# Kernel optimization log

Hardware: AMD Instinct MI355X
Metric: run time of the kernel (lower is better)

Reference implementation:

```python
import jax, jax.numpy as jnp
import numpy as np

B, N, OBS, HID, H = 8, 1024, 64, 192, 3
D = HID // H  # head_dim = 64
ALPHA = 0.2   # LeakyReLU negative slope
NEG = -9e15   # mask value from torch code (-9000000000000000.0)


def gat_layer(h, adj, W, a):
    """Multi-head GAT layer, math-identical to the torch per-head loop.
    h: (B,N,F_in), adj: (N,N), W: (H,F_in,D), a: (H,2D).
    Concat-score a^T [Wh_i || Wh_j] is split into a_l^T Wh_i + a_r^T Wh_j
    (broadcast-add) to avoid materializing the N^2 x 2D tensor.
    """
    Wh = jnp.einsum('bni,hid->bhnd', h, W)           # (B,H,N,D)
    d = Wh.shape[-1]
    s_i = jnp.einsum('bhnd,hd->bhn', Wh, a[:, :d])   # a_l . Wh_i
    s_j = jnp.einsum('bhnd,hd->bhn', Wh, a[:, d:])   # a_r . Wh_j
    e = s_i[..., :, None] + s_j[..., None, :]        # (B,H,N,N)
    e = jnp.where(e > 0, e, ALPHA * e)               # LeakyReLU
    e = jnp.where(adj > 0, e, NEG)                   # adjacency mask
    attn = jax.nn.softmax(e, axis=-1)                # (dropout=0 in eval)
    out = jnp.einsum('bhnm,bhmd->bhnd', attn, Wh)    # weighted aggregate
    b, nh, n, _ = out.shape
    return out.transpose(0, 2, 1, 3).reshape(b, n, nh * d)  # concat heads


def setup_inputs() -> dict:
    key = jax.random.key(0)
    k1, k2, k3, k4, k5 = jax.random.split(key, 5)
    h = jax.random.normal(k1, (B, N, OBS), dtype=jnp.float32)
    adj = jnp.ones((N, N), dtype=jnp.float32)  # graph_type='full'
    # xavier_uniform-style scale (gain=1.414)
    def xav(k, shape, fan_in, fan_out):
        lim = 1.414 * np.sqrt(6.0 / (fan_in + fan_out))
        return jax.random.uniform(k, shape, jnp.float32, -lim, lim)
    W1 = xav(k2, (H, OBS, D), OBS, D)
    a1 = xav(k3, (H, 2 * D), 2 * D, 1)
    W2 = xav(k4, (H, HID, D), HID, D)
    a2 = xav(k5, (H, 2 * D), 2 * D, 1)
    return {"h": h, "adj": adj, "W1": W1, "a1": a1, "W2": W2, "a2": a2}


def reference(h, adj, W1, a1, W2, a2):
    x = gat_layer(h, adj, W1, a1)   # (B,N,HID)
    x = jax.nn.elu(x)               # inter-layer nonlinearity
    x = gat_layer(x, adj, W2, a2)   # (B,N,HID)
    return x
```

## Files before the change

### kernel.cpp

```cpp
#include <hip/hip_runtime.h>
#include <math.h>

#define Bc   8
#define Nc   1024
#define OBSc 64
#define HIDc 192
#define NHc  3
#define Dc   64
#define ALPHAc 0.2f

typedef __attribute__((ext_vector_type(8))) _Float16 half8;
typedef __attribute__((ext_vector_type(4))) float floatx4;

__device__ __forceinline__ unsigned int enc_f32(float f) {
    unsigned int u = __float_as_uint(f);
    return (u & 0x80000000u) ? ~u : (u | 0x80000000u);
}
__device__ __forceinline__ float dec_f32(unsigned int e) {
    return __uint_as_float((e & 0x80000000u) ? (e & 0x7FFFFFFFu) : ~e);
}


__global__ __launch_bounds__(256) void proj1_kernel(
    const float* __restrict__ xin,
    const float* __restrict__ W1,
    const float* __restrict__ a,
    _Float16* __restrict__ WhT,
    float* __restrict__ si, float* __restrict__ sj,
    unsigned int* __restrict__ Menc,
    const float* __restrict__ adj,
    unsigned long long* __restrict__ adjb,
    const float* __restrict__ W2,
    _Float16* __restrict__ W2T)
{
    const int tid = threadIdx.x;
    const int bh  = blockIdx.y;

    if (bh == Bc * NHc) {
        const int px = blockIdx.x, wv = tid >> 6, lane = tid & 63;
        for (int r8 = 0; r8 < 8; ++r8) {
            const int i = px * 32 + wv * 8 + r8;
            unsigned long long word = 0;
            for (int g = 0; g < 16; ++g) {
                bool c = adj[(size_t)i * Nc + g * 64 + lane] > 0.f;
                unsigned long long bal = __ballot(c);
                if (lane == g) word = bal;
            }
            if (lane < 16) adjb[(size_t)i * 16 + lane] = word;
        }
        if (px < 12) {
            for (int e = px * 3072 + tid; e < px * 3072 + 3072; e += 256) {
                int t = e & 7, ln = (e >> 3) & 63, p = (e >> 9) & 1, nh = (e >> 10) & 1;
                int g = e >> 11; int ks = g % 6, hh = g / 6;
                int k = ks * 32 + (ln >> 4) * 8 + t;
                int d = nh * 32 + p * 16 + (ln & 15);
                W2T[e] = (_Float16)W2[((size_t)hh * HIDc + k) * Dc + d];
            }
        }
        return;
    }

    __shared__ union {
        _Float16 Bs[64][OBSc + 8];
        _Float16 Ts[64][40];
    } u;
    __shared__ float spsA_i[32], spsA_j[32], spsB_i[32], spsB_j[32];

    const int b = bh / NHc, hh = bh % NHc;
    const int row0 = blockIdx.x * 32;

    for (int e = tid; e < OBSc * 64; e += 256) {
        int k = e >> 6, d = e & 63;
        u.Bs[d][k] = (_Float16)W1[(size_t)hh * OBSc * 64 + e];
    }
    __syncthreads();

    const int lane = tid & 63, wv = tid >> 6;
    const int mblk = (wv & 1) * 16, nhalf = (wv >> 1) * 32;
    const int fr = lane & 15, fq = lane >> 4;
    floatx4 acc0 = {0.f,0.f,0.f,0.f}, acc1 = {0.f,0.f,0.f,0.f};
    const int row = row0 + mblk + fr;

#pragma unroll
    for (int ks = 0; ks < OBSc / 32; ++ks) {
        const int k0 = ks * 32 + fq * 8;
        const float* xr = xin + ((size_t)b * Nc + row) * OBSc + k0;
        float4 u0 = *(const float4*)xr;
        float4 u1 = *(const float4*)(xr + 4);
        half8 af;
        af[0] = (_Float16)u0.x; af[1] = (_Float16)u0.y;
        af[2] = (_Float16)u0.z; af[3] = (_Float16)u0.w;
        af[4] = (_Float16)u1.x; af[5] = (_Float16)u1.y;
        af[6] = (_Float16)u1.z; af[7] = (_Float16)u1.w;
        half8 b0 = *(const half8*)&u.Bs[nhalf + fr][k0];
        half8 b1 = *(const half8*)&u.Bs[nhalf + 16 + fr][k0];
        acc0 = __builtin_amdgcn_mfma_f32_16x16x32_f16(af, b0, acc0, 0, 0, 0);
        acc1 = __builtin_amdgcn_mfma_f32_16x16x32_f16(af, b1, acc1, 0, 0, 0);
    }

    const float al0 = a[hh * 2 * Dc + nhalf + fr];
    const float al1 = a[hh * 2 * Dc + nhalf + 16 + fr];
    const float ar0 = a[hh * 2 * Dc + Dc + nhalf + fr];
    const float ar1 = a[hh * 2 * Dc + Dc + nhalf + 16 + fr];
    float pi[4], pj[4];
#pragma unroll
    for (int r = 0; r < 4; ++r) {
        pi[r] = acc0[r] * al0 + acc1[r] * al1;
        pj[r] = acc0[r] * ar0 + acc1[r] * ar1;
        for (int off = 8; off >= 1; off >>= 1) {
            pi[r] += __shfl_xor(pi[r], off, 64);
            pj[r] += __shfl_xor(pj[r], off, 64);
        }
    }
    if (fr == 0) {
#pragma unroll
        for (int r = 0; r < 4; ++r) {
            int lr = mblk + fq * 4 + r;
            if (nhalf == 0) { spsA_i[lr] = pi[r]; spsA_j[lr] = pj[r]; }
            else            { spsB_i[lr] = pi[r]; spsB_j[lr] = pj[r]; }
        }
    }
    __syncthreads();
    if (tid < 64) {
        float vj = -INFINITY;
        if (tid < 32) {
            size_t g = (size_t)bh * Nc + row0 + tid;
            si[g] = spsA_i[tid] + spsB_i[tid];
            vj    = spsA_j[tid] + spsB_j[tid];
            sj[g] = vj;
        }
        float mv = vj;
        for (int off = 32; off >= 1; off >>= 1) mv = fmaxf(mv, __shfl_xor(mv, off, 64));
        if (tid == 0) atomicMax(&Menc[bh], enc_f32(mv));
    }

#pragma unroll
    for (int nt = 0; nt < 2; ++nt) {
        const int d = nhalf + nt * 16 + fr;
        floatx4 acc = nt ? acc1 : acc0;
#pragma unroll
        for (int p = 0; p < 2; ++p) {
            union { unsigned int w; _Float16 h[2]; } pk;
            pk.h[0] = (_Float16)acc[2 * p];
            pk.h[1] = (_Float16)acc[2 * p + 1];
            *(unsigned int*)&u.Ts[d][mblk + fq * 4 + 2 * p] = pk.w;
        }
    }
    __syncthreads();
    {
        const int c2 = tid >> 6, lane2 = tid & 63;
        const int fr2 = lane2 & 15, fq2 = lane2 >> 4;
        const int jt = row0 >> 5;
        uint4 v = *(const uint4*)&u.Ts[c2 * 16 + fr2][fq2 * 8];
        *(uint4*)&WhT[(size_t)(bh * 32 + jt) * 2048 + tid * 8] = v;
    }
}

__global__ __launch_bounds__(256) void proj2_kernel(
    const _Float16* __restrict__ xh,
    const _Float16* __restrict__ W2T,
    const float* __restrict__ a,
    _Float16* __restrict__ WhT,
    float* __restrict__ si, float* __restrict__ sj,
    unsigned int* __restrict__ Menc)
{
    __shared__ _Float16 Ts[64][40];
    __shared__ float spsA_i[32], spsA_j[32], spsB_i[32], spsB_j[32];

    const int tid = threadIdx.x, bh = blockIdx.y;
    const int b = bh / NHc, hh = bh % NHc;
    const int row0 = blockIdx.x * 32;
    const int lane = tid & 63, wv = tid >> 6;
    const int mblk = (wv & 1) * 16, nhalf = (wv >> 1) * 32;
    const int fr = lane & 15, fq = lane >> 4;
    const int nh = nhalf >> 5;

    floatx4 acc0 = {0.f,0.f,0.f,0.f}, acc1 = {0.f,0.f,0.f,0.f};
    const int row = row0 + mblk + fr;

#pragma unroll
    for (int ks = 0; ks < HIDc / 32; ++ks) {
        half8 af = *(const half8*)&xh[((size_t)b * Nc + row) * HIDc + ks * 32 + fq * 8];
        const _Float16* wb = W2T + (size_t)((hh * 6 + ks) * 2 + nh) * 1024 + lane * 8;
        half8 b0 = *(const half8*)wb;
        half8 b1 = *(const half8*)(wb + 512);
        acc0 = __builtin_amdgcn_mfma_f32_16x16x32_f16(af, b0, acc0, 0, 0, 0);
        acc1 = __builtin_amdgcn_mfma_f32_16x16x32_f16(af, b1, acc1, 0, 0, 0);
    }

    const float al0 = a[hh * 2 * Dc + nhalf + fr];
    const float al1 = a[hh * 2 * Dc + nhalf + 16 + fr];
    const float ar0 = a[hh * 2 * Dc + Dc + nhalf + fr];
    const float ar1 = a[hh * 2 * Dc + Dc + nhalf + 16 + fr];
    float pi[4], pj[4];
#pragma unroll
    for (int r = 0; r < 4; ++r) {
        pi[r] = acc0[r] * al0 + acc1[r] * al1;
        pj[r] = acc0[r] * ar0 + acc1[r] * ar1;
        for (int off = 8; off >= 1; off >>= 1) {
            pi[r] += __shfl_xor(pi[r], off, 64);
            pj[r] += __shfl_xor(pj[r], off, 64);
        }
    }
    if (fr == 0) {
#pragma unroll
        for (int r = 0; r < 4; ++r) {
            int lr = mblk + fq * 4 + r;
            if (nhalf == 0) { spsA_i[lr] = pi[r]; spsA_j[lr] = pj[r]; }
            else            { spsB_i[lr] = pi[r]; spsB_j[lr] = pj[r]; }
        }
    }
    __syncthreads();
    if (tid < 64) {
        float vj = -INFINITY;
        if (tid < 32) {
            size_t g = (size_t)bh * Nc + row0 + tid;
            si[g] = spsA_i[tid] + spsB_i[tid];
            vj    = spsA_j[tid] + spsB_j[tid];
            sj[g] = vj;
        }
        float mv = vj;
        for (int off = 32; off >= 1; off >>= 1) mv = fmaxf(mv, __shfl_xor(mv, off, 64));
        if (tid == 0) atomicMax(&Menc[bh], enc_f32(mv));
    }

#pragma unroll
    for (int nt = 0; nt < 2; ++nt) {
        const int d = nhalf + nt * 16 + fr;
        floatx4 acc = nt ? acc1 : acc0;
#pragma unroll
        for (int p = 0; p < 2; ++p) {
            union { unsigned int w; _Float16 h[2]; } pk;
            pk.h[0] = (_Float16)acc[2 * p];
            pk.h[1] = (_Float16)acc[2 * p + 1];
            *(unsigned int*)&Ts[d][mblk + fq * 4 + 2 * p] = pk.w;
        }
    }
    __syncthreads();
    {
        const int c2 = tid >> 6, lane2 = tid & 63;
        const int fr2 = lane2 & 15, fq2 = lane2 >> 4;
        const int jt = row0 >> 5;
        uint4 v = *(const uint4*)&Ts[c2 * 16 + fr2][fq2 * 8];
        *(uint4*)&WhT[(size_t)(bh * 32 + jt) * 2048 + tid * 8] = v;
    }
}

template <bool DO_ELU, typename OutT>
__global__ __launch_bounds__(256, 4) void aggr_kernel(
    const _Float16* __restrict__ WhT,
    const float* __restrict__ si,
    const float* __restrict__ sj,
    const unsigned int* __restrict__ Menc,
    const unsigned long long* __restrict__ adjb,
    OutT* __restrict__ out)
{
    __shared__ float red[4][64][20];
    __shared__ float zs[4][16];

    const int tid  = threadIdx.x;
    const int wv   = tid >> 6, lane = tid & 63;
    const int bh   = blockIdx.x >> 6;
    const int row0 = (blockIdx.x & 63) << 4;
    const int b    = bh / NHc, hh = bh % NHc;
    const int fr   = lane & 15, fq = lane >> 4;
    const int row  = row0 + fr;

    const float M   = dec_f32(Menc[bh]);
    const float s_i = si[(size_t)bh * Nc + row];
    const float em  = s_i + M;
    const float m_i = fmaxf(em, ALPHAc * em);

    const float* sjr = sj + (size_t)bh * Nc + fq * 8;
    const unsigned long long* arow = adjb + (size_t)row * 16;
    const _Float16* Bp = WhT + (size_t)bh * 65536 + (size_t)wv * 8 * 2048 + lane * 8;

    floatx4 acc[4] = {{0.f,0.f,0.f,0.f},{0.f,0.f,0.f,0.f},
                      {0.f,0.f,0.f,0.f},{0.f,0.f,0.f,0.f}};
    float zacc = 0.f;

    float4 sa = *(const float4*)&sjr[wv * 256];
    float4 sb = *(const float4*)&sjr[wv * 256 + 4];
    unsigned long long w = arow[(wv * 8) >> 1];
    half8 bfr0 = *(const half8*)(Bp);
    half8 bfr1 = *(const half8*)(Bp + 512);
    half8 bfr2 = *(const half8*)(Bp + 1024);
    half8 bfr3 = *(const half8*)(Bp + 1536);

#pragma unroll
    for (int s8 = 0; s8 < 8; ++s8) {
        const int s = wv * 8 + s8;
        float4 nsa, nsb; unsigned long long nw;
        half8 nb0, nb1, nb2, nb3;
        if (s8 < 7) {
            const int jn = (s + 1) * 32 - wv * 256;
            nsa = *(const float4*)&sjr[(s + 1) * 32];
            nsb = *(const float4*)&sjr[(s + 1) * 32 + 4];
            nw  = arow[(s + 1) >> 1];
            const _Float16* bn = Bp + (size_t)(s8 + 1) * 2048;
            nb0 = *(const half8*)(bn);
            nb1 = *(const half8*)(bn + 512);
            nb2 = *(const half8*)(bn + 1024);
            nb3 = *(const half8*)(bn + 1536);
            (void)jn;
        }
        const int bb = (s & 1) * 32 + fq * 8;
        const float sv[8] = {sa.x, sa.y, sa.z, sa.w, sb.x, sb.y, sb.z, sb.w};
        float p[8];
        if (w == ~0ULL) {
#pragma unroll
            for (int t = 0; t < 8; ++t) {
                float e = s_i + sv[t];
                e = fmaxf(e, ALPHAc * e) - m_i;
                p[t] = __expf(e);
            }
        } else {
#pragma unroll
            for (int t = 0; t < 8; ++t) {
                float e = s_i + sv[t];
                e = fmaxf(e, ALPHAc * e) - m_i;
                e = ((w >> (bb + t)) & 1) ? e : -1e30f;
                p[t] = __expf(e);
            }
        }
        zacc += ((p[0] + p[1]) + (p[2] + p[3])) + ((p[4] + p[5]) + (p[6] + p[7]));
        union { half8 v; _Float16 h[8]; } A;
#pragma unroll
        for (int t = 0; t < 8; ++t) A.h[t] = (_Float16)p[t];
        acc[0] = __builtin_amdgcn_mfma_f32_16x16x32_f16(A.v, bfr0, acc[0], 0, 0, 0);
        acc[1] = __builtin_amdgcn_mfma_f32_16x16x32_f16(A.v, bfr1, acc[1], 0, 0, 0);
        acc[2] = __builtin_amdgcn_mfma_f32_16x16x32_f16(A.v, bfr2, acc[2], 0, 0, 0);
        acc[3] = __builtin_amdgcn_mfma_f32_16x16x32_f16(A.v, bfr3, acc[3], 0, 0, 0);
        if (s8 < 7) {
            sa = nsa; sb = nsb; w = nw;
            bfr0 = nb0; bfr1 = nb1; bfr2 = nb2; bfr3 = nb3;
        }
    }

    zacc += __shfl_xor(zacc, 16, 64);
    zacc += __shfl_xor(zacc, 32, 64);
    if (lane < 16) zs[wv][lane] = zacc;
#pragma unroll
    for (int c = 0; c < 4; ++c)
        *(floatx4*)&red[wv][lane][c * 4] = acc[c];
    __syncthreads();

    floatx4 af = {0.f, 0.f, 0.f, 0.f};
#pragma unroll
    for (int w2 = 0; w2 < 4; ++w2) {
        floatx4 r = *(const floatx4*)&red[w2][lane][wv * 4];
        af[0] += r[0]; af[1] += r[1]; af[2] += r[2]; af[3] += r[3];
    }
#pragma unroll
    for (int reg = 0; reg < 4; ++reg) {
        const int r = fq * 4 + reg;
        const float Z = (zs[0][r] + zs[1][r]) + (zs[2][r] + zs[3][r]);
        float v = af[reg] / Z;
        if (DO_ELU) v = v > 0.f ? v : expm1f(v);
        out[((size_t)b * Nc + row0 + r) * HIDc + hh * Dc + wv * 16 + fr] = (OutT)v;
    }
}

extern "C" void kernel_launch(void* const* d_in, const int* in_sizes, int n_in,
                              void* d_out, int out_size, void* d_ws, size_t ws_size,
                              hipStream_t stream) {
    const float* h_in = (const float*)d_in[0];
    const float* adj  = (const float*)d_in[1];
    const float* W1   = (const float*)d_in[2];
    const float* a1   = (const float*)d_in[3];
    const float* W2   = (const float*)d_in[4];
    const float* a2   = (const float*)d_in[5];
    float* out = (float*)d_out;

    float* ws = (float*)d_ws;
    const size_t nWhT_f = (size_t)Bc * NHc * Dc * Nc / 2;
    const size_t nXh_f  = (size_t)Bc * Nc * HIDc / 2;
    const size_t nAb_f  = (size_t)Nc * 16 * 2;
    const size_t nW2T_f = 36864 / 2;
    const size_t nR     = (size_t)Bc * NHc * Nc;
    _Float16* WhT = (_Float16*)ws;
    _Float16* xh  = (_Float16*)(ws + nWhT_f);
    unsigned long long* adjb = (unsigned long long*)(ws + nWhT_f + nXh_f);
    _Float16* W2T = (_Float16*)(ws + nWhT_f + nXh_f + nAb_f);
    float* si = ws + nWhT_f + nXh_f + nAb_f + nW2T_f;
    float* sj = si + nR;
    unsigned int* Menc = (unsigned int*)(sj + nR);

    (void)hipMemsetAsync(Menc, 0, 48 * sizeof(unsigned int), stream);

    dim3 projGrid1(Nc / 32, Bc * NHc + 1);
    dim3 projGrid2(Nc / 32, Bc * NHc);

    proj1_kernel<<<projGrid1, 256, 0, stream>>>(
        h_in, W1, a1, WhT, si, sj, Menc, adj, adjb, W2, W2T);
    aggr_kernel<true, _Float16><<<1536, 256, 0, stream>>>(
        WhT, si, sj, Menc, adjb, xh);

    proj2_kernel<<<projGrid2, 256, 0, stream>>>(
        xh, W2T, a2, WhT, si, sj, Menc + 24);
    aggr_kernel<false, float><<<1536, 256, 0, stream>>>(
        WhT, si, sj, Menc + 24, adjb, out);
}
```

Baseline: 136.0 us.

## Fuse GAT pipeline into one cooperative persistent kernel with grid syncs

Merges the four kernels (proj1 plus aux, aggr1, proj2, aggr2) into one cooperative persistent kernel separated by grid-wide barriers, with a four-kernel fallback if the cooperative launch fails. The global atomicMax column-max and its memset are replaced by per-chunk partial maxima that each aggregation block reduces itself. The aggregation tile grows to 32 rows with a 2-way k split, halving aggregation blocks to 768. The aim is to remove launch gaps and the memset, at the cost of grid.sync overhead and fewer, longer-running blocks per phase.

Result: slower. 406.9 us (+199.2%).

```diff
diff --git a/kernel.cpp b/kernel.cpp
--- a/kernel.cpp
+++ b/kernel.cpp
@@ -1,5 +1,8 @@
 #include <hip/hip_runtime.h>
+#include <hip/hip_cooperative_groups.h>
 #include <math.h>
+
+namespace cg = cooperative_groups;
 
 #define Bc   8
 #define Nc   1024
@@ -8,70 +11,34 @@
 #define NHc  3
 #define Dc   64
 #define ALPHAc 0.2f
+#define UNITS 768
+#define AUXU  32
 
 typedef __attribute__((ext_vector_type(8))) _Float16 half8;
 typedef __attribute__((ext_vector_type(4))) float floatx4;
 
-__device__ __forceinline__ unsigned int enc_f32(float f) {
-    unsigned int u = __float_as_uint(f);
-    return (u & 0x80000000u) ? ~u : (u | 0x80000000u);
-}
-__device__ __forceinline__ float dec_f32(unsigned int e) {
-    return __uint_as_float((e & 0x80000000u) ? (e & 0x7FFFFFFFu) : ~e);
-}
-
-
-__global__ __launch_bounds__(256) void proj1_kernel(
-    const float* __restrict__ xin,
-    const float* __restrict__ W1,
-    const float* __restrict__ a,
-    _Float16* __restrict__ WhT,
-    float* __restrict__ si, float* __restrict__ sj,
-    unsigned int* __restrict__ Menc,
-    const float* __restrict__ adj,
-    unsigned long long* __restrict__ adjb,
-    const float* __restrict__ W2,
-    _Float16* __restrict__ W2T)
-{
-    const int tid = threadIdx.x;
-    const int bh  = blockIdx.y;
-
-    if (bh == Bc * NHc) {
-        const int px = blockIdx.x, wv = tid >> 6, lane = tid & 63;
-        for (int r8 = 0; r8 < 8; ++r8) {
-            const int i = px * 32 + wv * 8 + r8;
-            unsigned long long word = 0;
-            for (int g = 0; g < 16; ++g) {
-                bool c = adj[(size_t)i * Nc + g * 64 + lane] > 0.f;
-                unsigned long long bal = __ballot(c);
-                if (lane == g) word = bal;
-            }
-            if (lane < 16) adjb[(size_t)i * 16 + lane] = word;
-        }
-        if (px < 12) {
-            for (int e = px * 3072 + tid; e < px * 3072 + 3072; e += 256) {
-                int t = e & 7, ln = (e >> 3) & 63, p = (e >> 9) & 1, nh = (e >> 10) & 1;
-                int g = e >> 11; int ks = g % 6, hh = g / 6;
-                int k = ks * 32 + (ln >> 4) * 8 + t;
-                int d = nh * 32 + p * 16 + (ln & 15);
-                W2T[e] = (_Float16)W2[((size_t)hh * HIDc + k) * Dc + d];
-            }
-        }
-        return;
-    }
-
-    __shared__ union {
-        _Float16 Bs[64][OBSc + 8];
+struct SM {
+    union {
+        _Float16 Bs[64][72];
         _Float16 Ts[64][40];
+        struct { float red[4][64][20]; float zs[4][16]; } ag;
     } u;
-    __shared__ float spsA_i[32], spsA_j[32], spsB_i[32], spsB_j[32];
-
+    float spsAi[32], spsAj[32], spsBi[32], spsBj[32];
+};
+
+
+__device__ void proj1_block(int unit, int tid, SM* sm,
+    const float* __restrict__ xin, const float* __restrict__ W1,
+    const float* __restrict__ a1, _Float16* __restrict__ WhT,
+    float* __restrict__ si, float* __restrict__ sj, float* __restrict__ Mpart)
+{
+    const int bh = unit >> 5, chunk = unit & 31;
     const int b = bh / NHc, hh = bh % NHc;
-    const int row0 = blockIdx.x * 32;
+    const int row0 = chunk * 32;
 
     for (int e = tid; e < OBSc * 64; e += 256) {
         int k = e >> 6, d = e & 63;
-        u.Bs[d][k] = (_Float16)W1[(size_t)hh * OBSc * 64 + e];
+        sm->u.Bs[d][k] = (_Float16)W1[(size_t)hh * OBSc * 64 + e];
     }
     __syncthreads();
 
@@ -92,16 +59,16 @@
         af[2] = (_Float16)u0.z; af[3] = (_Float16)u0.w;
         af[4] = (_Float16)u1.x; af[5] = (_Float16)u1.y;
         af[6] = (_Float16)u1.z; af[7] = (_Float16)u1.w;
-        half8 b0 = *(const half8*)&u.Bs[nhalf + fr][k0];
-        half8 b1 = *(const half8*)&u.Bs[nhalf + 16 + fr][k0];
+        half8 b0 = *(const half8*)&sm->u.Bs[nhalf + fr][k0];
+        half8 b1 = *(const half8*)&sm->u.Bs[nhalf + 16 + fr][k0];
         acc0 = __builtin_amdgcn_mfma_f32_16x16x32_f16(af, b0, acc0, 0, 0, 0);
         acc1 = __builtin_amdgcn_mfma_f32_16x16x32_f16(af, b1, acc1, 0, 0, 0);
     }
 
-    const float al0 = a[hh * 2 * Dc + nhalf + fr];
-    const float al1 = a[hh * 2 * Dc + nhalf + 16 + fr];
-    const float ar0 = a[hh * 2 * Dc + Dc + nhalf + fr];
-    const float ar1 = a[hh * 2 * Dc + Dc + nhalf + 16 + fr];
+    const float al0 = a1[hh * 2 * Dc + nhalf + fr];
+    const float al1 = a1[hh * 2 * Dc + nhalf + 16 + fr];
+    const float ar0 = a1[hh * 2 * Dc + Dc + nhalf + fr];
+    const float ar1 = a1[hh * 2 * Dc + Dc + nhalf + 16 + fr];
     float pi[4], pj[4];
 #pragma unroll
     for (int r = 0; r < 4; ++r) {
@@ -116,8 +83,8 @@
 #pragma unroll
         for (int r = 0; r < 4; ++r) {
             int lr = mblk + fq * 4 + r;
-            if (nhalf == 0) { spsA_i[lr] = pi[r]; spsA_j[lr] = pj[r]; }
-            else            { spsB_i[lr] = pi[r]; spsB_j[lr] = pj[r]; }
+            if (nhalf == 0) { sm->spsAi[lr] = pi[r]; sm->spsAj[lr] = pj[r]; }
+            else            { sm->spsBi[lr] = pi[r]; sm->spsBj[lr] = pj[r]; }
         }
     }
     __syncthreads();
@@ -125,13 +92,13 @@
         float vj = -INFINITY;
         if (tid < 32) {
             size_t g = (size_t)bh * Nc + row0 + tid;
-            si[g] = spsA_i[tid] + spsB_i[tid];
-            vj    = spsA_j[tid] + spsB_j[tid];
+            si[g] = sm->spsAi[tid] + sm->spsBi[tid];
+            vj    = sm->spsAj[tid] + sm->spsBj[tid];
             sj[g] = vj;
         }
         float mv = vj;
         for (int off = 32; off >= 1; off >>= 1) mv = fmaxf(mv, __shfl_xor(mv, off, 64));
-        if (tid == 0) atomicMax(&Menc[bh], enc_f32(mv));
+        if (tid == 0) Mpart[bh * 32 + chunk] = mv;
     }
 
 #pragma unroll
@@ -143,33 +110,53 @@
             union { unsigned int w; _Float16 h[2]; } pk;
             pk.h[0] = (_Float16)acc[2 * p];
             pk.h[1] = (_Float16)acc[2 * p + 1];
-            *(unsigned int*)&u.Ts[d][mblk + fq * 4 + 2 * p] = pk.w;
+            *(unsigned int*)&sm->u.Ts[d][mblk + fq * 4 + 2 * p] = pk.w;
         }
     }
     __syncthreads();
     {
         const int c2 = tid >> 6, lane2 = tid & 63;
         const int fr2 = lane2 & 15, fq2 = lane2 >> 4;
-        const int jt = row0 >> 5;
-        uint4 v = *(const uint4*)&u.Ts[c2 * 16 + fr2][fq2 * 8];
-        *(uint4*)&WhT[(size_t)(bh * 32 + jt) * 2048 + tid * 8] = v;
-    }
-}
-
-__global__ __launch_bounds__(256) void proj2_kernel(
-    const _Float16* __restrict__ xh,
-    const _Float16* __restrict__ W2T,
-    const float* __restrict__ a,
-    _Float16* __restrict__ WhT,
-    float* __restrict__ si, float* __restrict__ sj,
-    unsigned int* __restrict__ Menc)
-{
-    __shared__ _Float16 Ts[64][40];
-    __shared__ float spsA_i[32], spsA_j[32], spsB_i[32], spsB_j[32];
-
-    const int tid = threadIdx.x, bh = blockIdx.y;
+        uint4 v = *(const uint4*)&sm->u.Ts[c2 * 16 + fr2][fq2 * 8];
+        *(uint4*)&WhT[(size_t)(bh * 32 + chunk) * 2048 + tid * 8] = v;
+    }
+    __syncthreads();
+}
+
+__device__ void aux_block(int px, int tid,
+    const float* __restrict__ adj, unsigned long long* __restrict__ adjb,
+    const float* __restrict__ W2, _Float16* __restrict__ W2T)
+{
+    const int wv = tid >> 6, lane = tid & 63;
+    for (int r8 = 0; r8 < 8; ++r8) {
+        const int i = px * 32 + wv * 8 + r8;
+        unsigned long long word = 0;
+        for (int g = 0; g < 16; ++g) {
+            bool c = adj[(size_t)i * Nc + g * 64 + lane] > 0.f;
+            unsigned long long bal = __ballot(c);
+            if (lane == g) word = bal;
+        }
+        if (lane < 16) adjb[(size_t)i * 16 + lane] = word;
+    }
+    if (px < 12) {
+        for (int e = px * 3072 + tid; e < px * 3072 + 3072; e += 256) {
+            int t = e & 7, ln = (e >> 3) & 63, p = (e >> 9) & 1, nh = (e >> 10) & 1;
+            int gg = e >> 11; int ks = gg % 6, hh = gg / 6;
+            int k = ks * 32 + (ln >> 4) * 8 + t;
+            int d = nh * 32 + p * 16 + (ln & 15);
+            W2T[e] = (_Float16)W2[((size_t)hh * HIDc + k) * Dc + d];
+        }
+    }
+}
+
+__device__ void proj2_block(int unit, int tid, SM* sm,
+    const _Float16* __restrict__ xh, const _Float16* __restrict__ W2T,
+    const float* __restrict__ a2, _Float16* __restrict__ WhT,
+    float* __restrict__ si, float* __restrict__ sj, float* __restrict__ Mpart)
+{
+    const int bh = unit >> 5, chunk = unit & 31;
     const int b = bh / NHc, hh = bh % NHc;
-    const int row0 = blockIdx.x * 32;
+    const int row0 = chunk * 32;
     const int lane = tid & 63, wv = tid >> 6;
     const int mblk = (wv & 1) * 16, nhalf = (wv >> 1) * 32;
     const int fr = lane & 15, fq = lane >> 4;
@@ -188,10 +175,10 @@
         acc1 = __builtin_amdgcn_mfma_f32_16x16x32_f16(af, b1, acc1, 0, 0, 0);
     }
 
-    const float al0 = a[hh * 2 * Dc + nhalf + fr];
-    const float al1 = a[hh * 2 * Dc + nhalf + 16 + fr];
-    const float ar0 = a[hh * 2 * Dc + Dc + nhalf + fr];
-    const float ar1 = a[hh * 2 * Dc + Dc + nhalf + 16 + fr];
+    const float al0 = a2[hh * 2 * Dc + nhalf + fr];
+    const float al1 = a2[hh * 2 * Dc + nhalf + 16 + fr];
+    const float ar0 = a2[hh * 2 * Dc + Dc + nhalf + fr];
+    const float ar1 = a2[hh * 2 * Dc + Dc + nhalf + 16 + fr];
     float pi[4], pj[4];
 #pragma unroll
     for (int r = 0; r < 4; ++r) {
@@ -206,8 +193,8 @@
 #pragma unroll
         for (int r = 0; r < 4; ++r) {
             int lr = mblk + fq * 4 + r;
-            if (nhalf == 0) { spsA_i[lr] = pi[r]; spsA_j[lr] = pj[r]; }
-            else            { spsB_i[lr] = pi[r]; spsB_j[lr] = pj[r]; }
+            if (nhalf == 0) { sm->spsAi[lr] = pi[r]; sm->spsAj[lr] = pj[r]; }
+            else            { sm->spsBi[lr] = pi[r]; sm->spsBj[lr] = pj[r]; }
         }
     }
     __syncthreads();
@@ -215,13 +202,13 @@
         float vj = -INFINITY;
         if (tid < 32) {
             size_t g = (size_t)bh * Nc + row0 + tid;
-            si[g] = spsA_i[tid] + spsB_i[tid];
-            vj    = spsA_j[tid] + spsB_j[tid];
+            si[g] = sm->spsAi[tid] + sm->spsBi[tid];
+            vj    = sm->spsAj[tid] + sm->spsBj[tid];
             sj[g] = vj;
         }
         float mv = vj;
         for (int off = 32; off >= 1; off >>= 1) mv = fmaxf(mv, __shfl_xor(mv, off, 64));
-        if (tid == 0) atomicMax(&Menc[bh], enc_f32(mv));
+        if (tid == 0) Mpart[bh * 32 + chunk] = mv;
     }
 
 #pragma unroll
@@ -233,76 +220,72 @@
             union { unsigned int w; _Float16 h[2]; } pk;
             pk.h[0] = (_Float16)acc[2 * p];
             pk.h[1] = (_Float16)acc[2 * p + 1];
-            *(unsigned int*)&Ts[d][mblk + fq * 4 + 2 * p] = pk.w;
+            *(unsigned int*)&sm->u.Ts[d][mblk + fq * 4 + 2 * p] = pk.w;
         }
     }
     __syncthreads();
     {
         const int c2 = tid >> 6, lane2 = tid & 63;
         const int fr2 = lane2 & 15, fq2 = lane2 >> 4;
-        const int jt = row0 >> 5;
-        uint4 v = *(const uint4*)&Ts[c2 * 16 + fr2][fq2 * 8];
-        *(uint4*)&WhT[(size_t)(bh * 32 + jt) * 2048 + tid * 8] = v;
-    }
+        uint4 v = *(const uint4*)&sm->u.Ts[c2 * 16 + fr2][fq2 * 8];
+        *(uint4*)&WhT[(size_t)(bh * 32 + chunk) * 2048 + tid * 8] = v;
+    }
+    __syncthreads();
 }
 
 template <bool DO_ELU, typename OutT>
-__global__ __launch_bounds__(256, 4) void aggr_kernel(
-    const _Float16* __restrict__ WhT,
-    const float* __restrict__ si,
-    const float* __restrict__ sj,
-    const unsigned int* __restrict__ Menc,
-    const unsigned long long* __restrict__ adjb,
-    OutT* __restrict__ out)
-{
-    __shared__ float red[4][64][20];
-    __shared__ float zs[4][16];
-
-    const int tid  = threadIdx.x;
-    const int wv   = tid >> 6, lane = tid & 63;
-    const int bh   = blockIdx.x >> 6;
-    const int row0 = (blockIdx.x & 63) << 4;
-    const int b    = bh / NHc, hh = bh % NHc;
-    const int fr   = lane & 15, fq = lane >> 4;
-    const int row  = row0 + fr;
-
-    const float M   = dec_f32(Menc[bh]);
+__device__ void aggr_block(int unit, int tid, SM* sm,
+    const _Float16* __restrict__ WhT, const float* __restrict__ si,
+    const float* __restrict__ sj, const float* __restrict__ Mpart,
+    const unsigned long long* __restrict__ adjb, OutT* __restrict__ outp)
+{
+    const int wv = tid >> 6, lane = tid & 63;
+    const int bh = unit >> 5;
+    const int row0 = (unit & 31) << 5;
+    const int b = bh / NHc, hh = bh % NHc;
+    const int fr = lane & 15, fq = lane >> 4;
+    const int g  = wv >> 1;
+    const int kh = wv & 1;
+    const int row = row0 + g * 16 + fr;
+
+    float mpv = Mpart[bh * 32 + (lane & 31)];
+    for (int off = 16; off >= 1; off >>= 1) mpv = fmaxf(mpv, __shfl_xor(mpv, off, 64));
+
     const float s_i = si[(size_t)bh * Nc + row];
-    const float em  = s_i + M;
+    const float em  = s_i + mpv;
     const float m_i = fmaxf(em, ALPHAc * em);
 
-    const float* sjr = sj + (size_t)bh * Nc + fq * 8;
+    const float* sjr = sj + (size_t)bh * Nc;
     const unsigned long long* arow = adjb + (size_t)row * 16;
-    const _Float16* Bp = WhT + (size_t)bh * 65536 + (size_t)wv * 8 * 2048 + lane * 8;
+    const _Float16* Bp = WhT + (size_t)bh * 65536 + (size_t)kh * 32768 + lane * 8;
 
     floatx4 acc[4] = {{0.f,0.f,0.f,0.f},{0.f,0.f,0.f,0.f},
                       {0.f,0.f,0.f,0.f},{0.f,0.f,0.f,0.f}};
     float zacc = 0.f;
 
-    float4 sa = *(const float4*)&sjr[wv * 256];
-    float4 sb = *(const float4*)&sjr[wv * 256 + 4];
-    unsigned long long w = arow[(wv * 8) >> 1];
+    float4 sa = *(const float4*)&sjr[(kh * 16) * 32 + fq * 8];
+    float4 sb = *(const float4*)&sjr[(kh * 16) * 32 + fq * 8 + 4];
+    unsigned long long w = arow[(kh * 16) >> 1];
     half8 bfr0 = *(const half8*)(Bp);
     half8 bfr1 = *(const half8*)(Bp + 512);
     half8 bfr2 = *(const half8*)(Bp + 1024);
     half8 bfr3 = *(const half8*)(Bp + 1536);
 
 #pragma unroll
-    for (int s8 = 0; s8 < 8; ++s8) {
-        const int s = wv * 8 + s8;
+    for (int s16 = 0; s16 < 16; ++s16) {
+        const int s = kh * 16 + s16;
         float4 nsa, nsb; unsigned long long nw;
         half8 nb0, nb1, nb2, nb3;
-        if (s8 < 7) {
-            const int jn = (s + 1) * 32 - wv * 256;
-            nsa = *(const float4*)&sjr[(s + 1) * 32];
-            nsb = *(const float4*)&sjr[(s + 1) * 32 + 4];
+        if (s16 < 15) {
+            const int jn = (s + 1) * 32 + fq * 8;
+            nsa = *(const float4*)&sjr[jn];
+            nsb = *(const float4*)&sjr[jn + 4];
             nw  = arow[(s + 1) >> 1];
-            const _Float16* bn = Bp + (size_t)(s8 + 1) * 2048;
+            const _Float16* bn = Bp + (size_t)(s16 + 1) * 2048;
             nb0 = *(const half8*)(bn);
             nb1 = *(const half8*)(bn + 512);
             nb2 = *(const half8*)(bn + 1024);
             nb3 = *(const half8*)(bn + 1536);
-            (void)jn;
         }
         const int bb = (s & 1) * 32 + fq * 8;
         const float sv[8] = {sa.x, sa.y, sa.z, sa.w, sb.x, sb.y, sb.z, sb.w};
@@ -331,7 +314,7 @@
         acc[1] = __builtin_amdgcn_mfma_f32_16x16x32_f16(A.v, bfr1, acc[1], 0, 0, 0);
         acc[2] = __builtin_amdgcn_mfma_f32_16x16x32_f16(A.v, bfr2, acc[2], 0, 0, 0);
         acc[3] = __builtin_amdgcn_mfma_f32_16x16x32_f16(A.v, bfr3, acc[3], 0, 0, 0);
-        if (s8 < 7) {
+        if (s16 < 15) {
             sa = nsa; sb = nsb; w = nw;
             bfr0 = nb0; bfr1 = nb1; bfr2 = nb2; bfr3 = nb3;
         }
@@ -339,26 +322,96 @@
 
     zacc += __shfl_xor(zacc, 16, 64);
     zacc += __shfl_xor(zacc, 32, 64);
-    if (lane < 16) zs[wv][lane] = zacc;
+    if (lane < 16) sm->u.ag.zs[wv][lane] = zacc;
 #pragma unroll
     for (int c = 0; c < 4; ++c)
-        *(floatx4*)&red[wv][lane][c * 4] = acc[c];
-    __syncthreads();
-
-    floatx4 af = {0.f, 0.f, 0.f, 0.f};
-#pragma unroll
-    for (int w2 = 0; w2 < 4; ++w2) {
-        floatx4 r = *(const floatx4*)&red[w2][lane][wv * 4];
-        af[0] += r[0]; af[1] += r[1]; af[2] += r[2]; af[3] += r[3];
-    }
-#pragma unroll
-    for (int reg = 0; reg < 4; ++reg) {
-        const int r = fq * 4 + reg;
-        const float Z = (zs[0][r] + zs[1][r]) + (zs[2][r] + zs[3][r]);
-        float v = af[reg] / Z;
-        if (DO_ELU) v = v > 0.f ? v : expm1f(v);
-        out[((size_t)b * Nc + row0 + r) * HIDc + hh * Dc + wv * 16 + fr] = (OutT)v;
-    }
+        *(floatx4*)&sm->u.ag.red[wv][lane][c * 4] = acc[c];
+    __syncthreads();
+
+    const int w0 = g * 2;
+#pragma unroll
+    for (int cc = 0; cc < 2; ++cc) {
+        const int c = kh * 2 + cc;
+        floatx4 af;
+#pragma unroll
+        for (int reg = 0; reg < 4; ++reg)
+            af[reg] = sm->u.ag.red[w0][lane][c * 4 + reg]
+                    + sm->u.ag.red[w0 + 1][lane][c * 4 + reg];
+#pragma unroll
+        for (int reg = 0; reg < 4; ++reg) {
+            const int r = fq * 4 + reg;
+            const float Z = sm->u.ag.zs[w0][r] + sm->u.ag.zs[w0 + 1][r];
+            float v = af[reg] / Z;
+            if (DO_ELU) v = v > 0.f ? v : expm1f(v);
+            outp[((size_t)b * Nc + row0 + g * 16 + r) * HIDc + hh * Dc + c * 16 + fr] = (OutT)v;
+        }
+    }
+    __syncthreads();
+}
+
+__global__ __launch_bounds__(256, 3) void gat_mega(
+    const float* __restrict__ xin, const float* __restrict__ adj,
+    const float* __restrict__ W1, const float* __restrict__ a1,
+    const float* __restrict__ W2, const float* __restrict__ a2,
+    float* __restrict__ out,
+    _Float16* __restrict__ WhT1, _Float16* __restrict__ WhT2,
+    _Float16* __restrict__ xh, unsigned long long* __restrict__ adjb,
+    _Float16* __restrict__ W2T,
+    float* __restrict__ si1, float* __restrict__ sj1,
+    float* __restrict__ si2, float* __restrict__ sj2,
+    float* __restrict__ Mp1, float* __restrict__ Mp2)
+{
+    __shared__ SM sm;
+    const int tid = threadIdx.x;
+    cg::grid_group grid = cg::this_grid();
+
+    for (int u = blockIdx.x; u < UNITS + AUXU; u += gridDim.x) {
+        if (u < UNITS) proj1_block(u, tid, &sm, xin, W1, a1, WhT1, si1, sj1, Mp1);
+        else           aux_block(u - UNITS, tid, adj, adjb, W2, W2T);
+    }
+    __threadfence(); grid.sync(); __threadfence();
+
+    for (int u = blockIdx.x; u < UNITS; u += gridDim.x)
+        aggr_block<true, _Float16>(u, tid, &sm, WhT1, si1, sj1, Mp1, adjb, xh);
+    __threadfence(); grid.sync(); __threadfence();
+
+    for (int u = blockIdx.x; u < UNITS; u += gridDim.x)
+        proj2_block(u, tid, &sm, xh, W2T, a2, WhT2, si2, sj2, Mp2);
+    __threadfence(); grid.sync(); __threadfence();
+
+    for (int u = blockIdx.x; u < UNITS; u += gridDim.x)
+        aggr_block<false, float>(u, tid, &sm, WhT2, si2, sj2, Mp2, adjb, out);
+}
+
+__global__ __launch_bounds__(256, 3) void k_phase1(
+    const float* xin, const float* adj, const float* W1, const float* a1,
+    const float* W2, _Float16* WhT1, _Float16* W2T,
+    unsigned long long* adjb, float* si, float* sj, float* Mp)
+{
+    __shared__ SM sm;
+    if (blockIdx.x < UNITS) proj1_block(blockIdx.x, threadIdx.x, &sm, xin, W1, a1, WhT1, si, sj, Mp);
+    else                    aux_block(blockIdx.x - UNITS, threadIdx.x, adj, adjb, W2, W2T);
+}
+__global__ __launch_bounds__(256, 3) void k_aggr1(
+    const _Float16* WhT, const float* si, const float* sj, const float* Mp,
+    const unsigned long long* adjb, _Float16* xh)
+{
+    __shared__ SM sm;
+    aggr_block<true, _Float16>(blockIdx.x, threadIdx.x, &sm, WhT, si, sj, Mp, adjb, xh);
+}
+__global__ __launch_bounds__(256, 3) void k_proj2(
+    const _Float16* xh, const _Float16* W2T, const float* a2,
+    _Float16* WhT2, float* si, float* sj, float* Mp)
+{
+    __shared__ SM sm;
+    proj2_block(blockIdx.x, threadIdx.x, &sm, xh, W2T, a2, WhT2, si, sj, Mp);
+}
+__global__ __launch_bounds__(256, 3) void k_aggr2(
+    const _Float16* WhT, const float* si, const float* sj, const float* Mp,
+    const unsigned long long* adjb, float* out)
+{
+    __shared__ SM sm;
+    aggr_block<false, float>(blockIdx.x, threadIdx.x, &sm, WhT, si, sj, Mp, adjb, out);
 }
 
 extern "C" void kernel_launch(void* const* d_in, const int* in_sizes, int n_in,
@@ -378,26 +431,41 @@
     const size_t nAb_f  = (size_t)Nc * 16 * 2;
     const size_t nW2T_f = 36864 / 2;
     const size_t nR     = (size_t)Bc * NHc * Nc;
-    _Float16* WhT = (_Float16*)ws;
-    _Float16* xh  = (_Float16*)(ws + nWhT_f);
-    unsigned long long* adjb = (unsigned long long*)(ws + nWhT_f + nXh_f);
-    _Float16* W2T = (_Float16*)(ws + nWhT_f + nXh_f + nAb_f);
-    float* si = ws + nWhT_f + nXh_f + nAb_f + nW2T_f;
-    float* sj = si + nR;
-    unsigned int* Menc = (unsigned int*)(sj + nR);
-
-    (void)hipMemsetAsync(Menc, 0, 48 * sizeof(unsigned int), stream);
-
-    dim3 projGrid1(Nc / 32, Bc * NHc + 1);
-    dim3 projGrid2(Nc / 32, Bc * NHc);
-
-    proj1_kernel<<<projGrid1, 256, 0, stream>>>(
-        h_in, W1, a1, WhT, si, sj, Menc, adj, adjb, W2, W2T);
-    aggr_kernel<true, _Float16><<<1536, 256, 0, stream>>>(
-        WhT, si, sj, Menc, adjb, xh);
-
-    proj2_kernel<<<projGrid2, 256, 0, stream>>>(
-        xh, W2T, a2, WhT, si, sj, Menc + 24);
-    aggr_kernel<false, float><<<1536, 256, 0, stream>>>(
-        WhT, si, sj, Menc + 24, adjb, out);
-}
+    _Float16* WhT1 = (_Float16*)ws;
+    _Float16* WhT2 = (_Float16*)(ws + nWhT_f);
+    _Float16* xh   = (_Float16*)(ws + 2 * nWhT_f);
+    unsigned long long* adjb = (unsigned long long*)(ws + 2 * nWhT_f + nXh_f);
+    _Float16* W2T  = (_Float16*)(ws + 2 * nWhT_f + nXh_f + nAb_f);
+    float* si1 = ws + 2 * nWhT_f + nXh_f + nAb_f + nW2T_f;
+    float* sj1 = si1 + nR;
+    float* si2 = sj1 + nR;
+    float* sj2 = si2 + nR;
+    float* Mp1 = sj2 + nR;
+    float* Mp2 = Mp1 + UNITS;
+
+    int dev = 0, cus = 256, nb = 0;
+    (void)hipGetDevice(&dev);
+    (void)hipDeviceGetAttribute(&cus, hipDeviceAttributeMultiprocessorCount, dev);
+    (void)hipOccupancyMaxActiveBlocksPerMultiprocessor(&nb, gat_mega, 256, 0);
+    int grid = nb * cus;
+    if (grid > UNITS + AUXU) grid = UNITS + AUXU;
+
+    hipError_t err = hipErrorUnknown;
+    if (grid >= 64) {
+        void* kargs[] = {
+            (void*)&h_in, (void*)&adj, (void*)&W1, (void*)&a1, (void*)&W2, (void*)&a2,
+            (void*)&out, (void*)&WhT1, (void*)&WhT2, (void*)&xh, (void*)&adjb,
+            (void*)&W2T, (void*)&si1, (void*)&sj1, (void*)&si2, (void*)&sj2,
+            (void*)&Mp1, (void*)&Mp2
+        };
+        err = hipLaunchCooperativeKernel((void*)gat_mega, dim3(grid), dim3(256),
+                                         kargs, 0, stream);
+    }
+    if (err != hipSuccess) {
+        k_phase1<<<UNITS + AUXU, 256, 0, stream>>>(h_in, adj, W1, a1, W2,
+                                                   WhT1, W2T, adjb, si1, sj1, Mp1);
+        k_aggr1<<<UNITS, 256, 0, stream>>>(WhT1, si1, sj1, Mp1, adjb, xh);
+        k_proj2<<<UNITS, 256, 0, stream>>>(xh, W2T, a2, WhT2, si2, sj2, Mp2);
+        k_aggr2<<<UNITS, 256, 0, stream>>>(WhT2, si2, sj2, Mp2, adjb, out);
+    }
+}
```
